# Performance work log

Measured on AMD Instinct MI355X. Metric: run time of the kernel, lower is better.

Reference implementation:

```python
import jax, jax.numpy as jnp
import numpy as np

N_NODES = 100000

def setup_inputs() -> dict:
    key = jax.random.key(0)
    k1, k2 = jax.random.split(key)
    x = jax.random.normal(k1, (N_NODES, 48), dtype=jnp.float32)
    edge_index = jax.random.randint(k2, (2, 1600000), 0, N_NODES, dtype=jnp.int64)
    return {"x": x, "edge_index": edge_index}

def reference(x, edge_index):
    # adj = SparseTensor.from_edge_index(edge_index): row=edge_index[0], col=edge_index[1]
    # adj.matmul(x): out[i] = sum over edges with row==i of x[col]
    row, col = edge_index[0], edge_index[1]
    x_neighbors_sum = jax.ops.segment_sum(x[col], row, num_segments=x.shape[0])  # [N, D]
    node_labels = jnp.concatenate((x, x_neighbors_sum), axis=-1)  # [N, 2D]
    return node_labels
```

## Files before the change

kernel.cpp:

```cpp
#include <hip/hip_runtime.h>


constexpr int D_IN  = 48;
constexpr int BSH   = 7;
constexpr int BNODES = 1 << BSH;
constexpr int MAXNB = 1024;
constexpr int CAPB  = 2400;
constexpr int OVF_MAX = 4096;

constexpr int PT_THREADS = 256;
constexpr int PT_ITEMS   = 16;
constexpr int PT_TILE    = PT_THREADS * PT_ITEMS;

constexpr int AG_THREADS = 512;
constexpr int AG_ITEMS   = 5;


__device__ __forceinline__ unsigned int bf16rne(float f) {
    unsigned int u = __float_as_uint(f);
    return (u + 0x7fffu + ((u >> 16) & 1u)) >> 16;
}
__device__ __forceinline__ unsigned int packbf(float a, float b) {
    return bf16rne(a) | (bf16rne(b) << 16);
}
__device__ __forceinline__ void accbf(float4& a, uint2 u) {
    a.x += __uint_as_float(u.x << 16);
    a.y += __uint_as_float(u.x & 0xffff0000u);
    a.z += __uint_as_float(u.y << 16);
    a.w += __uint_as_float(u.y & 0xffff0000u);
}
__device__ __forceinline__ void add4(float4& a, const float4& b) {
    a.x += b.x; a.y += b.y; a.z += b.z; a.w += b.w;
}


__global__ __launch_bounds__(PT_THREADS)
void prep_kernel(const int* __restrict__ row, const int* __restrict__ col,
                 int* __restrict__ gcursor, unsigned int* __restrict__ pairs,
                 int* __restrict__ ovf_cnt, uint2* __restrict__ ovf,
                 const float4* __restrict__ x4, uint4* __restrict__ x2u4,
                 float4* __restrict__ out4,
                 int n_edges, int nb, int ntiles, int n_nodes) {
    __shared__ int hist[MAXNB];
    __shared__ int offs[MAXNB];
    __shared__ int gbase[MAXNB];
    __shared__ int scanbuf[PT_THREADS];

    int t = threadIdx.x;

    if (blockIdx.x >= ntiles) {
        int i = (blockIdx.x - ntiles) * PT_THREADS + t;
        if (i < n_nodes * 6) {
            int n = i / 6, s = i - n * 6;
            float4 v0 = x4[(size_t)n * 12 + 2 * s];
            float4 v1 = x4[(size_t)n * 12 + 2 * s + 1];
            out4[(size_t)n * 24 + 2 * s]     = v0;
            out4[(size_t)n * 24 + 2 * s + 1] = v1;
            x2u4[(size_t)n * 6 + s] =
                make_uint4(packbf(v0.x, v0.y), packbf(v0.z, v0.w),
                           packbf(v1.x, v1.y), packbf(v1.z, v1.w));
        }
        return;
    }

    int tile0 = blockIdx.x * PT_TILE;

    for (int i = t; i < nb; i += PT_THREADS) hist[i] = 0;
    __syncthreads();

    int r[PT_ITEMS], c[PT_ITEMS];
#pragma unroll
    for (int j = 0; j < PT_ITEMS; ++j) {
        int e = tile0 + j * PT_THREADS + t;
        if (e < n_edges) {
            r[j] = row[e];
            c[j] = col[e];
            atomicAdd(&hist[r[j] >> BSH], 1);
        } else {
            r[j] = -1;
        }
    }
    __syncthreads();

    int cb = t * 4;
    int loc[4];
    int s = 0;
#pragma unroll
    for (int j = 0; j < 4; ++j) {
        int i = cb + j;
        loc[j] = (i < nb) ? hist[i] : 0;
        s += loc[j];
    }
    scanbuf[t] = s;
    __syncthreads();
    for (int off = 1; off < PT_THREADS; off <<= 1) {
        int v = (t >= off) ? scanbuf[t - off] : 0;
        __syncthreads();
        scanbuf[t] += v;
        __syncthreads();
    }
    int run = (t == 0) ? 0 : scanbuf[t - 1];
#pragma unroll
    for (int j = 0; j < 4; ++j) {
        int i = cb + j;
        if (i < nb) { offs[i] = run; run += loc[j]; }
    }
    __syncthreads();

    for (int i = t; i < nb; i += PT_THREADS) {
        int cnt = hist[i];
        gbase[i] = cnt ? (atomicAdd(&gcursor[i], cnt) - offs[i]) : 0;
        hist[i] = offs[i];
    }
    __syncthreads();

#pragma unroll
    for (int j = 0; j < PT_ITEMS; ++j) {
        if (r[j] >= 0) {
            int b = r[j] >> BSH;
            int lpos = atomicAdd(&hist[b], 1);
            int g = gbase[b] + lpos;
            if (g < CAPB) {
                pairs[(size_t)b * CAPB + g] =
                    ((unsigned int)(r[j] & (BNODES - 1)) << 17) | (unsigned int)c[j];
            } else {
                int o = atomicAdd(ovf_cnt, 1);
                if (o < OVF_MAX)
                    ovf[o] = make_uint2((unsigned int)r[j], (unsigned int)c[j]);
            }
        }
    }
}


template <int USE_BF16>
__global__ __launch_bounds__(AG_THREADS)
void agg_kernel(const float4* __restrict__ x4, const uint2* __restrict__ xbv,
                const unsigned int* __restrict__ pairs,
                const int* __restrict__ gcursor,
                const int* __restrict__ ovf_cnt, const uint2* __restrict__ ovf,
                float4* __restrict__ out4, int n_nodes) {
    __shared__ unsigned int scol[CAPB];
    __shared__ int hist[BNODES];
    __shared__ int offs[BNODES];
    __shared__ int cur[BNODES];
    __shared__ int hs[BNODES];

    int t   = threadIdx.x;
    int bkt = blockIdx.x;
    int cnt = min(gcursor[bkt], CAPB);
    const unsigned int* pb = pairs + (size_t)bkt * CAPB;

    if (t < BNODES) hist[t] = 0;
    __syncthreads();

    unsigned int pv[AG_ITEMS];
#pragma unroll
    for (int j = 0; j < AG_ITEMS; ++j) {
        int idx = t + j * AG_THREADS;
        if (idx < cnt) {
            pv[j] = pb[idx];
            atomicAdd(&hist[pv[j] >> 17], 1);
        }
    }
    __syncthreads();

    if (t < BNODES) hs[t] = hist[t];
    __syncthreads();
    for (int off = 1; off < BNODES; off <<= 1) {
        int v = (t >= off && t < BNODES) ? hs[t - off] : 0;
        __syncthreads();
        if (t < BNODES) hs[t] += v;
        __syncthreads();
    }
    if (t < BNODES) {
        offs[t] = hs[t] - hist[t];
        cur[t]  = offs[t];
    }
    __syncthreads();

#pragma unroll
    for (int j = 0; j < AG_ITEMS; ++j) {
        int idx = t + j * AG_THREADS;
        if (idx < cnt) {
            int pos = atomicAdd(&cur[pv[j] >> 17], 1);
            scol[pos] = pv[j] & 0x1FFFFu;
        }
    }
    __syncthreads();

    int n  = t >> 2;
    int qt = t & 3;
    float4 a0 = make_float4(0.f, 0.f, 0.f, 0.f);
    float4 a1 = make_float4(0.f, 0.f, 0.f, 0.f);
    float4 a2 = make_float4(0.f, 0.f, 0.f, 0.f);

    int k0 = offs[n];
    int k1 = k0 + hist[n];
    int k  = k0;
    if constexpr (USE_BF16) {
        for (; k + 4 <= k1; k += 4) {
            const uint2* pA = xbv + (size_t)scol[k]     * 12 + qt * 3;
            const uint2* pB = xbv + (size_t)scol[k + 1] * 12 + qt * 3;
            const uint2* pC = xbv + (size_t)scol[k + 2] * 12 + qt * 3;
            const uint2* pD = xbv + (size_t)scol[k + 3] * 12 + qt * 3;
            uint2 A0 = pA[0], A1 = pA[1], A2 = pA[2];
            uint2 B0 = pB[0], B1 = pB[1], B2 = pB[2];
            uint2 C0 = pC[0], C1 = pC[1], C2 = pC[2];
            uint2 D0 = pD[0], D1 = pD[1], D2 = pD[2];
            accbf(a0, A0); accbf(a1, A1); accbf(a2, A2);
            accbf(a0, B0); accbf(a1, B1); accbf(a2, B2);
            accbf(a0, C0); accbf(a1, C1); accbf(a2, C2);
            accbf(a0, D0); accbf(a1, D1); accbf(a2, D2);
        }
        for (; k < k1; ++k) {
            const uint2* p0 = xbv + (size_t)scol[k] * 12 + qt * 3;
            accbf(a0, p0[0]); accbf(a1, p0[1]); accbf(a2, p0[2]);
        }
    } else {
        for (; k + 2 <= k1; k += 2) {
            size_t c0 = (size_t)scol[k]     * 12 + qt * 3;
            size_t c1 = (size_t)scol[k + 1] * 12 + qt * 3;
            float4 u0 = x4[c0], u1 = x4[c0 + 1], u2 = x4[c0 + 2];
            float4 w0 = x4[c1], w1 = x4[c1 + 1], w2 = x4[c1 + 2];
            add4(a0, u0); add4(a1, u1); add4(a2, u2);
            add4(a0, w0); add4(a1, w1); add4(a2, w2);
        }
        if (k < k1) {
            size_t c0 = (size_t)scol[k] * 12 + qt * 3;
            add4(a0, x4[c0]); add4(a1, x4[c0 + 1]); add4(a2, x4[c0 + 2]);
        }
    }

    int oc = min(*ovf_cnt, OVF_MAX);
    for (int i = 0; i < oc; ++i) {
        uint2 rc = ovf[i];
        if ((int)(rc.x >> BSH) == bkt && (int)(rc.x & (BNODES - 1)) == n) {
            const float4* xr = x4 + (size_t)rc.y * 12 + qt * 3;
            add4(a0, xr[0]); add4(a1, xr[1]); add4(a2, xr[2]);
        }
    }

    int node = (bkt << BSH) + n;
    if (node < n_nodes) {
        size_t ob = (size_t)node * 24;
        out4[ob + 12 + qt * 3 + 0] = a0;
        out4[ob + 12 + qt * 3 + 1] = a1;
        out4[ob + 12 + qt * 3 + 2] = a2;
        if constexpr (!USE_BF16) {
            size_t xb = (size_t)node * 12;
            out4[ob + qt * 3 + 0] = x4[xb + qt * 3 + 0];
            out4[ob + qt * 3 + 1] = x4[xb + qt * 3 + 1];
            out4[ob + qt * 3 + 2] = x4[xb + qt * 3 + 2];
        }
    }
}


__global__ void init_out_kernel(const float4* __restrict__ x4,
                                float4* __restrict__ out4, int n_nodes) {
    int idx = blockIdx.x * blockDim.x + threadIdx.x;
    int total = n_nodes * 24;
    if (idx >= total) return;
    int i = idx / 24;
    int q = idx - i * 24;
    out4[idx] = (q < 12) ? x4[i * 12 + q] : make_float4(0.f, 0.f, 0.f, 0.f);
}

__global__ void scatter_add_kernel(const float* __restrict__ x,
                                   const int* __restrict__ row,
                                   const int* __restrict__ col,
                                   float* __restrict__ out, int n_edges) {
    long long gid = (long long)blockIdx.x * blockDim.x + threadIdx.x;
    long long total = (long long)n_edges * D_IN;
    if (gid >= total) return;
    int e = (int)(gid / D_IN);
    int d = (int)(gid - (long long)e * D_IN);
    atomicAdd(out + (long long)row[e] * 96 + D_IN + d,
              x[(long long)col[e] * D_IN + d]);
}


extern "C" void kernel_launch(void* const* d_in, const int* in_sizes, int n_in,
                              void* d_out, int out_size, void* d_ws, size_t ws_size,
                              hipStream_t stream) {
    const float* x  = (const float*)d_in[0];
    const int*   ei = (const int*)d_in[1];
    float*       out = (float*)d_out;

    int n_nodes = in_sizes[0] / D_IN;
    int n_edges = in_sizes[1] / 2;
    const int* row = ei;
    const int* col = ei + n_edges;

    int nb = (n_nodes + BNODES - 1) >> BSH;
    int ntiles = (n_edges + PT_TILE - 1) / PT_TILE;
    bool col_fits = n_nodes <= (1 << 17);

    size_t t2_bytes = ((size_t)nb * CAPB + nb + 1 + 2 * (size_t)OVF_MAX) * 4;
    size_t x2_off   = (t2_bytes + 15) & ~(size_t)15;
    size_t t1_bytes = x2_off + (size_t)n_nodes * 96;

    if (nb > MAXNB || !col_fits || ws_size < t2_bytes) {
        int init_total = n_nodes * 24;
        init_out_kernel<<<(init_total + 255) / 256, 256, 0, stream>>>(
            (const float4*)x, (float4*)out, n_nodes);
        long long total = (long long)n_edges * D_IN;
        scatter_add_kernel<<<(int)((total + 255) / 256), 256, 0, stream>>>(
            x, row, col, out, n_edges);
        return;
    }

    unsigned int* pairs = (unsigned int*)d_ws;
    int* gcursor = (int*)(pairs + (size_t)nb * CAPB);
    int* ovf_cnt = gcursor + nb;
    uint2* ovf   = (uint2*)(ovf_cnt + 1);
    bool bf16_tier = (ws_size >= t1_bytes);
    uint4* x2u4  = (uint4*)((char*)d_ws + x2_off);

    hipMemsetAsync(gcursor, 0, (size_t)(nb + 1) * sizeof(int), stream);

    int conv_blocks = bf16_tier ? (n_nodes * 6 + PT_THREADS - 1) / PT_THREADS : 0;
    prep_kernel<<<ntiles + conv_blocks, PT_THREADS, 0, stream>>>(
        row, col, gcursor, pairs, ovf_cnt, ovf,
        (const float4*)x, x2u4, (float4*)out, n_edges, nb, ntiles, n_nodes);

    if (bf16_tier) {
        agg_kernel<1><<<nb, AG_THREADS, 0, stream>>>(
            (const float4*)x, (const uint2*)x2u4, pairs, gcursor,
            ovf_cnt, ovf, (float4*)out, n_nodes);
    } else {
        agg_kernel<0><<<nb, AG_THREADS, 0, stream>>>(
            (const float4*)x, nullptr, pairs, gcursor,
            ovf_cnt, ovf, (float4*)out, n_nodes);
    }
}
```

Before: 85.32 us.

## Rework prep and aggregation scans, sort nodes by degree, shrink unroll

The prep kernel now handles 32 edges per thread and re-reads row/col in the scatter pass instead of keeping them in registers, and its block scan becomes a wavefront shuffle scan plus a cross-wave sum. The aggregation kernel replaces its shared-memory scan with a shuffle scan and counting-sorts nodes by degree so that neighbouring quads in a wavefront get similar trip counts. The bf16 gather loop unroll drops from 4 to 2. The intent is to cut barrier and register overhead and to reduce wavefront divergence, at the cost of reading edge indices twice and having less memory-level parallelism in the gather.

```diff
diff --git a/kernel.cpp b/kernel.cpp
--- a/kernel.cpp
+++ b/kernel.cpp
@@ -9,7 +9,7 @@
 constexpr int OVF_MAX = 4096;
 
 constexpr int PT_THREADS = 256;
-constexpr int PT_ITEMS   = 16;
+constexpr int PT_ITEMS   = 32;
 constexpr int PT_TILE    = PT_THREADS * PT_ITEMS;
 
 constexpr int AG_THREADS = 512;
@@ -44,7 +44,7 @@
     __shared__ int hist[MAXNB];
     __shared__ int offs[MAXNB];
     __shared__ int gbase[MAXNB];
-    __shared__ int scanbuf[PT_THREADS];
+    __shared__ int wsum[PT_THREADS / 64];
 
     int t = threadIdx.x;
 
@@ -68,17 +68,10 @@
     for (int i = t; i < nb; i += PT_THREADS) hist[i] = 0;
     __syncthreads();
 
-    int r[PT_ITEMS], c[PT_ITEMS];
-#pragma unroll
+#pragma unroll 8
     for (int j = 0; j < PT_ITEMS; ++j) {
         int e = tile0 + j * PT_THREADS + t;
-        if (e < n_edges) {
-            r[j] = row[e];
-            c[j] = col[e];
-            atomicAdd(&hist[r[j] >> BSH], 1);
-        } else {
-            r[j] = -1;
-        }
+        if (e < n_edges) atomicAdd(&hist[row[e] >> BSH], 1);
     }
     __syncthreads();
 
@@ -91,15 +84,19 @@
         loc[j] = (i < nb) ? hist[i] : 0;
         s += loc[j];
     }
-    scanbuf[t] = s;
-    __syncthreads();
-    for (int off = 1; off < PT_THREADS; off <<= 1) {
-        int v = (t >= off) ? scanbuf[t - off] : 0;
-        __syncthreads();
-        scanbuf[t] += v;
-        __syncthreads();
-    }
-    int run = (t == 0) ? 0 : scanbuf[t - 1];
+    int sc = s;
+#pragma unroll
+    for (int o = 1; o < 64; o <<= 1) {
+        int u = __shfl_up(sc, o);
+        if ((t & 63) >= o) sc += u;
+    }
+    if ((t & 63) == 63) wsum[t >> 6] = sc;
+    __syncthreads();
+    int wpre = 0;
+#pragma unroll
+    for (int w = 0; w < PT_THREADS / 64; ++w)
+        if (w < (t >> 6)) wpre += wsum[w];
+    int run = wpre + sc - s;
 #pragma unroll
     for (int j = 0; j < 4; ++j) {
         int i = cb + j;
@@ -114,19 +111,21 @@
     }
     __syncthreads();
 
-#pragma unroll
+#pragma unroll 8
     for (int j = 0; j < PT_ITEMS; ++j) {
-        if (r[j] >= 0) {
-            int b = r[j] >> BSH;
+        int e = tile0 + j * PT_THREADS + t;
+        if (e < n_edges) {
+            int r = row[e], c = col[e];
+            int b = r >> BSH;
             int lpos = atomicAdd(&hist[b], 1);
             int g = gbase[b] + lpos;
             if (g < CAPB) {
                 pairs[(size_t)b * CAPB + g] =
-                    ((unsigned int)(r[j] & (BNODES - 1)) << 17) | (unsigned int)c[j];
+                    ((unsigned int)(r & (BNODES - 1)) << 17) | (unsigned int)c;
             } else {
                 int o = atomicAdd(ovf_cnt, 1);
                 if (o < OVF_MAX)
-                    ovf[o] = make_uint2((unsigned int)r[j], (unsigned int)c[j]);
+                    ovf[o] = make_uint2((unsigned int)r, (unsigned int)c);
             }
         }
     }
@@ -144,7 +143,10 @@
     __shared__ int hist[BNODES];
     __shared__ int offs[BNODES];
     __shared__ int cur[BNODES];
-    __shared__ int hs[BNODES];
+    __shared__ int perm[BNODES];
+    __shared__ int dh[64];
+    __shared__ int dcur[64];
+    __shared__ int wtot;
 
     int t   = threadIdx.x;
     int bkt = blockIdx.x;
@@ -152,6 +154,7 @@
     const unsigned int* pb = pairs + (size_t)bkt * CAPB;
 
     if (t < BNODES) hist[t] = 0;
+    if (t < 64) dh[t] = 0;
     __syncthreads();
 
     unsigned int pv[AG_ITEMS];
@@ -165,17 +168,30 @@
     }
     __syncthreads();
 
-    if (t < BNODES) hs[t] = hist[t];
-    __syncthreads();
-    for (int off = 1; off < BNODES; off <<= 1) {
-        int v = (t >= off && t < BNODES) ? hs[t - off] : 0;
-        __syncthreads();
-        if (t < BNODES) hs[t] += v;
-        __syncthreads();
-    }
+    int v = (t < BNODES) ? hist[t] : 0;
+    int sc = v;
+#pragma unroll
+    for (int o = 1; o < 64; o <<= 1) {
+        int u = __shfl_up(sc, o);
+        if ((t & 63) >= o) sc += u;
+    }
+    if (t == 63) wtot = sc;
+    if (t < BNODES) atomicAdd(&dh[min(v, 63)], 1);
+    __syncthreads();
     if (t < BNODES) {
-        offs[t] = hs[t] - hist[t];
-        cur[t]  = offs[t];
+        int excl = sc - v + ((t >= 64) ? wtot : 0);
+        offs[t] = excl;
+        cur[t]  = excl;
+    }
+    {
+        int dv = (t < 64) ? dh[t] : 0;
+        int dsc = dv;
+#pragma unroll
+        for (int o = 1; o < 64; o <<= 1) {
+            int u = __shfl_up(dsc, o);
+            if ((t & 63) >= o) dsc += u;
+        }
+        if (t < 64) dcur[t] = dsc - dv;
     }
     __syncthreads();
 
@@ -187,9 +203,13 @@
             scol[pos] = pv[j] & 0x1FFFFu;
         }
     }
-    __syncthreads();
-
-    int n  = t >> 2;
+    if (t < BNODES) {
+        int slot = atomicAdd(&dcur[min(hist[t], 63)], 1);
+        perm[slot] = t;
+    }
+    __syncthreads();
+
+    int n  = perm[t >> 2];
     int qt = t & 3;
     float4 a0 = make_float4(0.f, 0.f, 0.f, 0.f);
     float4 a1 = make_float4(0.f, 0.f, 0.f, 0.f);
@@ -199,21 +219,15 @@
     int k1 = k0 + hist[n];
     int k  = k0;
     if constexpr (USE_BF16) {
-        for (; k + 4 <= k1; k += 4) {
+        for (; k + 2 <= k1; k += 2) {
             const uint2* pA = xbv + (size_t)scol[k]     * 12 + qt * 3;
             const uint2* pB = xbv + (size_t)scol[k + 1] * 12 + qt * 3;
-            const uint2* pC = xbv + (size_t)scol[k + 2] * 12 + qt * 3;
-            const uint2* pD = xbv + (size_t)scol[k + 3] * 12 + qt * 3;
             uint2 A0 = pA[0], A1 = pA[1], A2 = pA[2];
             uint2 B0 = pB[0], B1 = pB[1], B2 = pB[2];
-            uint2 C0 = pC[0], C1 = pC[1], C2 = pC[2];
-            uint2 D0 = pD[0], D1 = pD[1], D2 = pD[2];
             accbf(a0, A0); accbf(a1, A1); accbf(a2, A2);
             accbf(a0, B0); accbf(a1, B1); accbf(a2, B2);
-            accbf(a0, C0); accbf(a1, C1); accbf(a2, C2);
-            accbf(a0, D0); accbf(a1, D1); accbf(a2, D2);
-        }
-        for (; k < k1; ++k) {
+        }
+        if (k < k1) {
             const uint2* p0 = xbv + (size_t)scol[k] * 12 + qt * 3;
             accbf(a0, p0[0]); accbf(a1, p0[1]); accbf(a2, p0[2]);
         }
```

Result: slower. 87.71 us (+2.8%).
